# Kernel tuning notes

Measured on AMD Instinct MI355X. Metric: run time of the kernel, lower is better.

Reference implementation:

```python
import jax, jax.numpy as jnp
import numpy as np

N = 102400      # total agents across all groups
GROUP = 50      # agents per group
G = N // GROUP  # 2048 groups
E = 128         # embedding_dim
H = 512         # h_dim


def setup_inputs() -> dict:
    key = jax.random.key(0)
    k1, k2, k3, k4, k5, k6 = jax.random.split(key, 6)
    hist_enc = jax.random.normal(k1, (N, H), dtype=jnp.float32)
    hist_pos_batch = jax.random.normal(k2, (N, 2), dtype=jnp.float32)
    # group boundaries: 0, 50, 100, ..., N  (len = G+1)
    seq_start_end = (jnp.arange(G + 1, dtype=jnp.int32) * GROUP)
    # spatial_embedding: Linear(2, E)
    Ws = jax.random.normal(k3, (2, E), dtype=jnp.float32) * (1.0 / np.sqrt(2.0))
    bs = jax.random.normal(k4, (E,), dtype=jnp.float32) * 0.01
    # mlp_pre_pool: Linear(E + H, H)
    Wm = jax.random.normal(k5, (E + H, H), dtype=jnp.float32) * (1.0 / np.sqrt(E + H))
    bm = jax.random.normal(k6, (H,), dtype=jnp.float32) * 0.01
    return {
        "hist_enc": hist_enc,
        "hist_pos_batch": hist_pos_batch,
        "seq_start_end": seq_start_end,
        "Ws": Ws, "bs": bs, "Wm": Wm, "bm": bm,
    }


def reference(hist_enc, hist_pos_batch, seq_start_end, Ws, bs, Wm, bm):
    # The original torch loop builds all n^2 pairs per group but keeps only
    # curr_pool_h[0:1], i.e. row i=0 -> pooled vector for the group's FIRST agent.
    # rel[i=0, j] = pos[j] - pos[start]; hidden index is j; max over j.
    n = hist_enc.shape[0]
    num_groups = seq_start_end.shape[0] - 1
    # segment id of each agent: group g covers [sse[g], sse[g+1])
    seg_ids = jnp.searchsorted(seq_start_end, jnp.arange(n, dtype=seq_start_end.dtype), side="right") - 1
    starts = seq_start_end[:-1]                      # [G]
    anchor = hist_pos_batch[starts][seg_ids]         # [N,2] pos of group's first agent
    rel = hist_pos_batch - anchor                    # [N,2]
    emb = jax.nn.relu(rel @ Ws + bs)                 # [N,E]
    h_in = jnp.concatenate([hist_enc, emb], axis=1)  # [N,E+H]
    pooled = jax.nn.relu(h_in @ Wm + bm)             # [N,H]
    out = jax.ops.segment_max(pooled, seg_ids, num_segments=num_groups)  # [G,H]
    return out
```

## Files before the change

### kernel.cpp

```cpp
#include <hip/hip_runtime.h>


typedef __bf16 bf16x8 __attribute__((ext_vector_type(8)));
typedef float floatx4 __attribute__((ext_vector_type(4)));

constexpr int NR = 102400;
constexpr int NG = 2048;
constexpr int E  = 128;
constexpr int H  = 512;
constexpr int KD = 640;
constexpr int BM = 128, BN = 128, BK = 32;
constexpr int NKT = KD / BK;
constexpr int KH  = H / BK;

__device__ inline unsigned short f2bf(float f) {
    unsigned u = __float_as_uint(f);
    u += 0x7FFF + ((u >> 16) & 1u);
    return (unsigned short)(u >> 16);
}

__device__ inline unsigned pk2(float lo, float hi) {
    return __builtin_amdgcn_perm(__float_as_uint(hi) + 0x8000u,
                                 __float_as_uint(lo) + 0x8000u, 0x07060302u);
}

__global__ __launch_bounds__(256) void prep3(
    const float* __restrict__ pos, const int* __restrict__ sse,
    const float* __restrict__ Wm, unsigned short* __restrict__ WmT,
    int* __restrict__ segArr, float* __restrict__ relA)
{
    const int b = blockIdx.x;
    const int t = threadIdx.x;
    __shared__ float tile[64][65];
    if (b < 400) {
        if (!segArr) return;
        const int i = b * 256 + t;
        int l = 0, r = NG + 1;
        while (l < r) { int m = (l + r) >> 1; if (sse[m] <= i) l = m + 1; else r = m; }
        const int g = l - 1;
        segArr[i] = g;
        const int a = sse[g];
        relA[2 * i + 0] = pos[2 * i + 0] - pos[2 * a + 0];
        relA[2 * i + 1] = pos[2 * i + 1] - pos[2 * a + 1];
    } else {
        const int bb = b - 400;
        const int kb = (bb % 10) * 64, nb = (bb / 10) * 64;
        const int tx = t & 63, tq = t >> 6;
#pragma unroll
        for (int i = 0; i < 16; ++i) {
            const int k = tq * 16 + i;
            tile[k][tx] = Wm[(size_t)(kb + k) * H + nb + tx];
        }
        __syncthreads();
#pragma unroll
        for (int i = 0; i < 16; ++i) {
            const int n = tq * 16 + i;
            WmT[(size_t)(nb + n) * KD + kb + tx] = f2bf(tile[tx][n]);
        }
    }
}

__global__ __launch_bounds__(256, 2) void pool_flip(
    const float* __restrict__ hist_enc,
    const int*   __restrict__ sse,
    const int*   __restrict__ segArr,
    const float* __restrict__ relA,
    const float* __restrict__ Ws,
    const float* __restrict__ bs,
    const unsigned short* __restrict__ WmT,
    const float* __restrict__ bm,
    float*       __restrict__ out)
{
    __shared__ __attribute__((aligned(16))) unsigned short As[NKT * 64 * 32];

    const int t   = threadIdx.x;
    const int bid = blockIdx.x;
    const int x       = bid & 7;
    const int r_      = bid >> 3;
    const int colTile = r_ & 1;
    const int chunk   = (r_ >> 1) * 8 + x;
    const int rowBase = chunk * 64;
    const int cTile   = colTile * 256;

    const int lane  = t & 63;
    const int wv    = t >> 6;
    const int lcol  = lane & 15;
    const int lquad = lane >> 4;
    const int cb    = cTile + wv * 64;

    const unsigned short* pB[4];
#pragma unroll
    for (int nt = 0; nt < 4; ++nt)
        pB[nt] = WmT + (size_t)(cb + nt * 16 + lcol) * KD + lquad * 8;

    uint4 sB[2][4];
#pragma unroll
    for (int nt = 0; nt < 4; ++nt) {
        sB[0][nt] = *(const uint4*)(pB[nt]);
        sB[1][nt] = *(const uint4*)(pB[nt] + BK);
    }

    {
        const int row  = t >> 2;
        const int phys = t & 3;
        const int swz  = (row >> 1) & 3;
        const float* src = hist_enc + (size_t)(rowBase + row) * H + phys * 8;
#pragma unroll
        for (int i = 0; i < 16; ++i) {
            const float4 f0 = *(const float4*)(src + i * 32);
            const float4 f1 = *(const float4*)(src + i * 32 + 4);
            uint4 u;
            u.x = pk2(f0.x, f0.y); u.y = pk2(f0.z, f0.w);
            u.z = pk2(f1.x, f1.y); u.w = pk2(f1.z, f1.w);
            *(uint4*)&As[i * 2048 + row * 32 + (phys ^ swz) * 8] = u;
        }
        const float2 rr = *(const float2*)&relA[2 * (size_t)(rowBase + row)];
#pragma unroll
        for (int i = 0; i < 4; ++i) {
            const int e0 = (phys + 4 * i) * 8;
            const float4 w0a = *(const float4*)&Ws[e0];
            const float4 w0b = *(const float4*)&Ws[e0 + 4];
            const float4 w1a = *(const float4*)&Ws[E + e0];
            const float4 w1b = *(const float4*)&Ws[E + e0 + 4];
            const float4 ba4 = *(const float4*)&bs[e0];
            const float4 bb4 = *(const float4*)&bs[e0 + 4];
            float4 fa, fb;
            fa.x = fmaxf(rr.x * w0a.x + rr.y * w1a.x + ba4.x, 0.f);
            fa.y = fmaxf(rr.x * w0a.y + rr.y * w1a.y + ba4.y, 0.f);
            fa.z = fmaxf(rr.x * w0a.z + rr.y * w1a.z + ba4.z, 0.f);
            fa.w = fmaxf(rr.x * w0a.w + rr.y * w1a.w + ba4.w, 0.f);
            fb.x = fmaxf(rr.x * w0b.x + rr.y * w1b.x + bb4.x, 0.f);
            fb.y = fmaxf(rr.x * w0b.y + rr.y * w1b.y + bb4.y, 0.f);
            fb.z = fmaxf(rr.x * w0b.z + rr.y * w1b.z + bb4.z, 0.f);
            fb.w = fmaxf(rr.x * w0b.w + rr.y * w1b.w + bb4.w, 0.f);
            uint4 u;
            u.x = pk2(fa.x, fa.y); u.y = pk2(fa.z, fa.w);
            u.z = pk2(fb.x, fb.y); u.w = pk2(fb.z, fb.w);
            *(uint4*)&As[(16 + i) * 2048 + row * 32 + (phys ^ swz) * 8] = u;
        }
    }

    float bias[4];
#pragma unroll
    for (int nt = 0; nt < 4; ++nt) bias[nt] = bm[cb + nt * 16 + lcol];
    const int s0 = segArr[rowBase];
    const int bA = sse[s0 + 1];
    const int bB = (s0 + 2 <= NG) ? sse[s0 + 2] : 0x7fffffff;

    __syncthreads();

    floatx4 acc[4][4];
#pragma unroll
    for (int m = 0; m < 4; ++m)
#pragma unroll
        for (int n = 0; n < 4; ++n) acc[m][n] = (floatx4){0.f, 0.f, 0.f, 0.f};

#pragma unroll
    for (int kt = 0; kt < NKT; ++kt) {
        bf16x8 af[4];
#pragma unroll
        for (int mt = 0; mt < 4; ++mt) {
            const int R  = mt * 16 + lcol;
            const int pc = lquad ^ ((R >> 1) & 3);
            af[mt] = *(const bf16x8*)&As[kt * 2048 + R * 32 + pc * 8];
        }
        bf16x8 bfr[4];
#pragma unroll
        for (int nt = 0; nt < 4; ++nt) {
            union { uint4 u; bf16x8 v; } c; c.u = sB[kt & 1][nt];
            bfr[nt] = c.v;
        }

        __builtin_amdgcn_s_setprio(1);
#pragma unroll
        for (int mt = 0; mt < 4; ++mt)
#pragma unroll
            for (int nt = 0; nt < 4; ++nt)
                acc[mt][nt] = __builtin_amdgcn_mfma_f32_16x16x32_bf16(af[mt], bfr[nt], acc[mt][nt], 0, 0, 0);
        __builtin_amdgcn_s_setprio(0);

        if (kt + 2 < NKT) {
#pragma unroll
            for (int nt = 0; nt < 4; ++nt)
                sB[kt & 1][nt] = *(const uint4*)(pB[nt] + (kt + 2) * BK);
        }
    }

    float pm0[4] = {0.f, 0.f, 0.f, 0.f};
    float pm1[4] = {0.f, 0.f, 0.f, 0.f};
    float pm2[4] = {0.f, 0.f, 0.f, 0.f};
#pragma unroll
    for (int nt = 0; nt < 4; ++nt) {
#pragma unroll
        for (int mt = 0; mt < 4; ++mt) {
#pragma unroll
            for (int rr = 0; rr < 4; ++rr) {
                const int rowAbs = rowBase + mt * 16 + lquad * 4 + rr;
                const float v = fmaxf(acc[mt][nt][rr] + bias[nt], 0.f);
                const bool geA = rowAbs >= bA;
                const bool geB = rowAbs >= bB;
                pm0[nt] = fmaxf(pm0[nt], (!geA)        ? v : 0.f);
                pm1[nt] = fmaxf(pm1[nt], (geA && !geB) ? v : 0.f);
                pm2[nt] = fmaxf(pm2[nt], (geB)         ? v : 0.f);
            }
        }
    }
#pragma unroll
    for (int s = 0; s < 3; ++s) {
#pragma unroll
        for (int nt = 0; nt < 4; ++nt) {
            float v = (s == 0) ? pm0[nt] : (s == 1) ? pm1[nt] : pm2[nt];
            v = fmaxf(v, __shfl_xor(v, 16));
            v = fmaxf(v, __shfl_xor(v, 32));
            if (lquad == 0 && v > 0.f) {
                float* dst = &out[(size_t)(s0 + s) * H + cb + nt * 16 + lcol];
                atomicMax((int*)dst, __float_as_int(v));
            }
        }
    }
}

constexpr int LDAF = 40;
__global__ __launch_bounds__(256) void pool_mfma_fb(
    const float* __restrict__ hist_enc, const float* __restrict__ pos,
    const int* __restrict__ sse, const float* __restrict__ Ws,
    const float* __restrict__ bs, const unsigned short* __restrict__ WmT,
    const float* __restrict__ bm, float* __restrict__ out)
{
    __shared__ __attribute__((aligned(16))) unsigned short Asf[BM][LDAF];
    __shared__ __attribute__((aligned(16))) unsigned short Bsb[BN][LDAF];
    __shared__ float relRow[BM][2];
    __shared__ int   segRow[BM];
    __shared__ int   bnd[3];
    __shared__ int   Pmax[4][BN + 4];

    const int t = threadIdx.x;
    const int cTile = blockIdx.x * BN;
    const int rowBase = blockIdx.y * BM;

    if (t < BM) {
        const int i = rowBase + t;
        int l = 0, r = NG + 1;
        while (l < r) { int m = (l + r) >> 1; if (sse[m] <= i) l = m + 1; else r = m; }
        const int g = l - 1;
        segRow[t] = g;
        const int a = sse[g];
        relRow[t][0] = pos[2 * i + 0] - pos[2 * a + 0];
        relRow[t][1] = pos[2 * i + 1] - pos[2 * a + 1];
    }
    if (t >= BM && t < BM + 3) bnd[t - BM] = BM;
    for (int idx = t; idx < 4 * (BN + 4); idx += 256) ((int*)Pmax)[idx] = 0;
    __syncthreads();
    if (t < BM - 1) {
        const int s0 = segRow[t], s1 = segRow[t + 1];
        if (s1 != s0) bnd[s1 - segRow[0] - 1] = t + 1;
    }

    const int lane = t & 63, wv = t >> 6;
    const int wr = (wv >> 1) * 64, wc = (wv & 1) * 64;
    const int lcol = lane & 15, lquad = lane >> 4;

    floatx4 acc[4][4];
#pragma unroll
    for (int m = 0; m < 4; ++m)
#pragma unroll
        for (int n = 0; n < 4; ++n) acc[m][n] = (floatx4){0.f, 0.f, 0.f, 0.f};

    for (int kt = 0; kt < KD / BK; ++kt) {
        const int k0 = kt * BK;
        float4 av[4]; uint4 bv[2];
        if (k0 < H) {
#pragma unroll
            for (int i = 0; i < 4; ++i) {
                const int idx = i * 256 + t;
                const int row = idx >> 3, kq = (idx & 7) * 4;
                av[i] = *(const float4*)&hist_enc[(size_t)(rowBase + row) * H + k0 + kq];
            }
        } else {
#pragma unroll
            for (int i = 0; i < 4; ++i) {
                const int idx = i * 256 + t;
                const int row = idx >> 3, kq = (idx & 7) * 4;
                const int e = k0 - H + kq;
                const float4 w0 = *(const float4*)&Ws[e];
                const float4 w1 = *(const float4*)&Ws[E + e];
                const float4 b4 = *(const float4*)&bs[e];
                const float r0 = relRow[row][0], r1 = relRow[row][1];
                av[i].x = fmaxf(r0 * w0.x + r1 * w1.x + b4.x, 0.f);
                av[i].y = fmaxf(r0 * w0.y + r1 * w1.y + b4.y, 0.f);
                av[i].z = fmaxf(r0 * w0.z + r1 * w1.z + b4.z, 0.f);
                av[i].w = fmaxf(r0 * w0.w + r1 * w1.w + b4.w, 0.f);
            }
        }
#pragma unroll
        for (int i = 0; i < 2; ++i) {
            const int idx = i * 256 + t;
            const int n = idx >> 2, q = idx & 3;
            bv[i] = *(const uint4*)&WmT[(size_t)(cTile + n) * KD + k0 + q * 8];
        }
        __syncthreads();
#pragma unroll
        for (int i = 0; i < 4; ++i) {
            const int idx = i * 256 + t;
            const int row = idx >> 3, kq = (idx & 7) * 4;
            ushort4 p;
            p.x = f2bf(av[i].x); p.y = f2bf(av[i].y);
            p.z = f2bf(av[i].z); p.w = f2bf(av[i].w);
            *(ushort4*)&Asf[row][kq] = p;
        }
#pragma unroll
        for (int i = 0; i < 2; ++i) {
            const int idx = i * 256 + t;
            const int n = idx >> 2, q = idx & 3;
            *(uint4*)&Bsb[n][q * 8] = bv[i];
        }
        __syncthreads();

        bf16x8 af[4], bfr[4];
#pragma unroll
        for (int mt = 0; mt < 4; ++mt)
            af[mt] = *(const bf16x8*)&Asf[wr + mt * 16 + lcol][lquad * 8];
#pragma unroll
        for (int nt = 0; nt < 4; ++nt)
            bfr[nt] = *(const bf16x8*)&Bsb[wc + nt * 16 + lcol][lquad * 8];
#pragma unroll
        for (int mt = 0; mt < 4; ++mt)
#pragma unroll
            for (int nt = 0; nt < 4; ++nt)
                acc[mt][nt] = __builtin_amdgcn_mfma_f32_16x16x32_bf16(af[mt], bfr[nt], acc[mt][nt], 0, 0, 0);
    }

    const int b0 = bnd[0], b1 = bnd[1], b2 = bnd[2];
    const int segBase = segRow[0];
#pragma unroll
    for (int nt = 0; nt < 4; ++nt) {
        const int col = wc + nt * 16 + lcol;
        const float bias = bm[cTile + col];
        float pm[4] = {0.f, 0.f, 0.f, 0.f};
#pragma unroll
        for (int mt = 0; mt < 4; ++mt) {
#pragma unroll
            for (int r = 0; r < 4; ++r) {
                const int lr = wr + mt * 16 + lquad * 4 + r;
                const int ls = (lr >= b0) + (lr >= b1) + (lr >= b2);
                const float v = fmaxf(acc[mt][nt][r] + bias, 0.f);
                pm[ls] = fmaxf(pm[ls], v);
            }
        }
#pragma unroll
        for (int ls = 0; ls < 4; ++ls)
            if (pm[ls] > 0.f) atomicMax(&Pmax[ls][col], __float_as_int(pm[ls]));
    }
    __syncthreads();
    for (int idx = t; idx < 4 * BN; idx += 256) {
        const int ls = idx >> 7, col = idx & 127;
        if (ls > 0 && bnd[ls - 1] >= BM) continue;
        const int seg = segBase + ls;
        const int v = Pmax[ls][col];
        const int gs = sse[seg], ge = sse[seg + 1];
        float* dst = &out[(size_t)seg * H + cTile + col];
        if (gs >= rowBase && ge <= rowBase + BM) *dst = __int_as_float(v);
        else atomicMax((int*)dst, v);
    }
}

extern "C" void kernel_launch(void* const* d_in, const int* in_sizes, int n_in,
                              void* d_out, int out_size, void* d_ws, size_t ws_size,
                              hipStream_t stream) {
    const float* hist_enc = (const float*)d_in[0];
    const float* pos      = (const float*)d_in[1];
    const int*   sse      = (const int*)  d_in[2];
    const float* Ws       = (const float*)d_in[3];
    const float* bs       = (const float*)d_in[4];
    const float* Wm       = (const float*)d_in[5];
    const float* bm       = (const float*)d_in[6];
    float*       out      = (float*)d_out;

    const size_t needWmT = (size_t)H * KD * 2;
    const size_t needSeg = (size_t)NR * 4;
    const size_t needRel = (size_t)NR * 2 * 4;
    unsigned short* WmT  = (unsigned short*)d_ws;
    int*            segA = (int*)  ((char*)d_ws + needWmT);
    float*          relA = (float*)((char*)d_ws + needWmT + needSeg);

    hipMemsetAsync(out, 0, (size_t)out_size * sizeof(float), stream);

    if (ws_size >= needWmT + needSeg + needRel) {
        prep3<<<480, 256, 0, stream>>>(pos, sse, Wm, WmT, segA, relA);
        pool_flip<<<3200, 256, 0, stream>>>(hist_enc, sse, segA, relA, Ws, bs, WmT, bm, out);
    } else {
        prep3<<<480, 256, 0, stream>>>(pos, sse, Wm, WmT, nullptr, nullptr);
        pool_mfma_fb<<<dim3(H / BN, NR / BM), 256, 0, stream>>>(hist_enc, pos, sse, Ws, bs, WmT, bm, out);
    }
}
```

Measured before the change: 409.9 us.

## Widen pool block to 512 threads covering all columns per row chunk

Each block now has eight waves that cover all 512 output columns for a 64-row chunk. Previously two blocks of four waves split the columns, so each chunk's A tile was converted and staged in LDS twice. The kernel launches 1600 blocks of 512 threads instead of 3200 blocks of 256, and the next B-fragment prefetch is issued before the MFMA block so its latency overlaps the math. The cost is more threads per block and tighter launch bounds, which may limit registers per thread and occupancy.

```diff
diff --git a/kernel.cpp b/kernel.cpp
--- a/kernel.cpp
+++ b/kernel.cpp
@@ -60,7 +60,7 @@
     }
 }
 
-__global__ __launch_bounds__(256, 2) void pool_flip(
+__global__ __launch_bounds__(512, 4) void pool_flip8(
     const float* __restrict__ hist_enc,
     const int*   __restrict__ sse,
     const int*   __restrict__ segArr,
@@ -75,18 +75,13 @@
 
     const int t   = threadIdx.x;
     const int bid = blockIdx.x;
-    const int x       = bid & 7;
-    const int r_      = bid >> 3;
-    const int colTile = r_ & 1;
-    const int chunk   = (r_ >> 1) * 8 + x;
-    const int rowBase = chunk * 64;
-    const int cTile   = colTile * 256;
+    const int rowBase = bid * 64;
 
     const int lane  = t & 63;
     const int wv    = t >> 6;
     const int lcol  = lane & 15;
     const int lquad = lane >> 4;
-    const int cb    = cTile + wv * 64;
+    const int cb    = wv * 64;
 
     const unsigned short* pB[4];
 #pragma unroll
@@ -101,23 +96,26 @@
     }
 
     {
-        const int row  = t >> 2;
-        const int phys = t & 3;
+        const int row  = t >> 3;
+        const int phys = t & 7;
         const int swz  = (row >> 1) & 3;
         const float* src = hist_enc + (size_t)(rowBase + row) * H + phys * 8;
 #pragma unroll
-        for (int i = 0; i < 16; ++i) {
-            const float4 f0 = *(const float4*)(src + i * 32);
-            const float4 f1 = *(const float4*)(src + i * 32 + 4);
+        for (int p = 0; p < 8; ++p) {
+            const int c8 = p * 8 + phys;
+            const float4 f0 = *(const float4*)(src + p * 64);
+            const float4 f1 = *(const float4*)(src + p * 64 + 4);
             uint4 u;
             u.x = pk2(f0.x, f0.y); u.y = pk2(f0.z, f0.w);
             u.z = pk2(f1.x, f1.y); u.w = pk2(f1.z, f1.w);
-            *(uint4*)&As[i * 2048 + row * 32 + (phys ^ swz) * 8] = u;
+            const int kt = c8 >> 2, slot = (c8 & 3) ^ swz;
+            *(uint4*)&As[kt * 2048 + row * 32 + slot * 8] = u;
         }
         const float2 rr = *(const float2*)&relA[2 * (size_t)(rowBase + row)];
 #pragma unroll
-        for (int i = 0; i < 4; ++i) {
-            const int e0 = (phys + 4 * i) * 8;
+        for (int p = 0; p < 2; ++p) {
+            const int ce = p * 8 + phys;
+            const int e0 = ce * 8;
             const float4 w0a = *(const float4*)&Ws[e0];
             const float4 w0b = *(const float4*)&Ws[e0 + 4];
             const float4 w1a = *(const float4*)&Ws[E + e0];
@@ -136,7 +134,8 @@
             uint4 u;
             u.x = pk2(fa.x, fa.y); u.y = pk2(fa.z, fa.w);
             u.z = pk2(fb.x, fb.y); u.w = pk2(fb.z, fb.w);
-            *(uint4*)&As[(16 + i) * 2048 + row * 32 + (phys ^ swz) * 8] = u;
+            const int slot = (ce & 3) ^ swz;
+            *(uint4*)&As[(16 + (ce >> 2)) * 2048 + row * 32 + slot * 8] = u;
         }
     }
 
@@ -170,6 +169,11 @@
             union { uint4 u; bf16x8 v; } c; c.u = sB[kt & 1][nt];
             bfr[nt] = c.v;
         }
+        if (kt + 2 < NKT) {
+#pragma unroll
+            for (int nt = 0; nt < 4; ++nt)
+                sB[kt & 1][nt] = *(const uint4*)(pB[nt] + (kt + 2) * BK);
+        }
 
         __builtin_amdgcn_s_setprio(1);
 #pragma unroll
@@ -178,12 +182,6 @@
             for (int nt = 0; nt < 4; ++nt)
                 acc[mt][nt] = __builtin_amdgcn_mfma_f32_16x16x32_bf16(af[mt], bfr[nt], acc[mt][nt], 0, 0, 0);
         __builtin_amdgcn_s_setprio(0);
-
-        if (kt + 2 < NKT) {
-#pragma unroll
-            for (int nt = 0; nt < 4; ++nt)
-                sB[kt & 1][nt] = *(const uint4*)(pB[nt] + (kt + 2) * BK);
-        }
     }
 
     float pm0[4] = {0.f, 0.f, 0.f, 0.f};
@@ -383,11 +381,11 @@
     int*            segA = (int*)  ((char*)d_ws + needWmT);
     float*          relA = (float*)((char*)d_ws + needWmT + needSeg);
 
-    hipMemsetAsync(out, 0, (size_t)out_size * sizeof(float), stream);
+    (void)hipMemsetAsync(out, 0, (size_t)out_size * sizeof(float), stream);
 
     if (ws_size >= needWmT + needSeg + needRel) {
         prep3<<<480, 256, 0, stream>>>(pos, sse, Wm, WmT, segA, relA);
-        pool_flip<<<3200, 256, 0, stream>>>(hist_enc, sse, segA, relA, Ws, bs, WmT, bm, out);
+        pool_flip8<<<NR / 64, 512, 0, stream>>>(hist_enc, sse, segA, relA, Ws, bs, WmT, bm, out);
     } else {
         prep3<<<480, 256, 0, stream>>>(pos, sse, Wm, WmT, nullptr, nullptr);
         pool_mfma_fb<<<dim3(H / BN, NR / BM), 256, 0, stream>>>(hist_enc, pos, sse, Ws, bs, WmT, bm, out);
```

Result: slower. 574.0 us (+40.0%).
